# Performance work log

Hardware: AMD Instinct MI355X
Metric: run time of the kernel (lower is better)

Reference implementation:

```python
import jax, jax.numpy as jnp
import numpy as np
from jax import lax

B, C_G, H, W = 2, 64, 240, 1216
NUM, K, IDX_REF = 8, 9, 4  # prop_kernel=3
PROP_TIME = 6


def conv3x3(x, w, b):
    y = lax.conv_general_dilated(x, w, (1, 1), ((1, 1), (1, 1)),
                                 dimension_numbers=('NCHW', 'OIHW', 'NCHW'))
    return y + b[None, :, None, None]


def bilinear_sample(img, y, x):
    """img: (B,H,W); y,x: (B,K,H,W) absolute coords; zero padding outside."""
    Hh, Ww = img.shape[1], img.shape[2]
    y0 = jnp.floor(y)
    x0 = jnp.floor(x)
    wy1, wx1 = y - y0, x - x0
    gather = jax.vmap(lambda im, a, b: im[a, b])
    out = jnp.zeros_like(y)
    for i, (yy, wy) in enumerate(((y0, 1.0 - wy1), (y0 + 1.0, wy1))):
        for j, (xx, wx) in enumerate(((x0, 1.0 - wx1), (x0 + 1.0, wx1))):
            valid = (yy >= 0) & (yy <= Hh - 1) & (xx >= 0) & (xx <= Ww - 1)
            yi = jnp.clip(yy, 0, Hh - 1).astype(jnp.int32)
            xi = jnp.clip(xx, 0, Ww - 1).astype(jnp.int32)
            v = gather(img, yi, xi)
            out = out + wy * wx * jnp.where(valid, v, 0.0)
    return out


def setup_inputs() -> dict:
    key = jax.random.key(0)
    ks = jax.random.split(key, 6)
    return {
        'initial_disp': jax.random.uniform(ks[0], (B, 1, H, W), jnp.float32) * 50.0,
        'occlus_mask': jax.random.uniform(ks[1], (B, 1, H, W), jnp.float32),
        'confidence': jax.random.uniform(ks[2], (B, 1, H, W), jnp.float32),
        'guidance_feature': jax.random.normal(ks[3], (B, C_G, H, W), jnp.float32),
        'conv_w': 0.05 * jax.random.normal(ks[4], (3 * NUM, C_G, 3, 3), jnp.float32),
        'conv_b': jnp.zeros((3 * NUM,), jnp.float32),
        'aff_scale_const': jnp.full((1,), 0.5 * NUM, jnp.float32),  # TGASS: gamma*num
    }


def nlspn_forward(initial_disp, occlus_mask, confidence, guidance_feature,
                  conv_w, conv_b, aff_scale_const):
    Bb, _, Hh, Ww = guidance_feature.shape
    oa = conv3x3(guidance_feature, conv_w, conv_b)          # (B, 3*num, H, W)
    o1, o2, aff = oa[:, :NUM], oa[:, NUM:2 * NUM], oa[:, 2 * NUM:]
    off = jnp.concatenate([o1, o2], axis=1).reshape(Bb, NUM, 2, Hh, Ww)
    zero = jnp.zeros((Bb, 1, 2, Hh, Ww), off.dtype)
    off = jnp.concatenate([off[:, :IDX_REF], zero, off[:, IDX_REF:]], axis=1)  # (B,9,2,H,W)

    # TGASS affinity
    aff = jnp.tanh(aff) / (aff_scale_const[0] + 1e-8)       # (B,8,H,W)

    gy = jnp.arange(Hh, dtype=jnp.float32)[None, None, :, None]
    gx = jnp.arange(Ww, dtype=jnp.float32)[None, None, None, :]

    # confidence sampling: 1x1 deform conv (w_conf=1, bias=0), detached offsets
    off_sg = lax.stop_gradient(off)
    nb = jnp.array([0, 1, 2, 3, 5, 6, 7, 8])
    conf_s = bilinear_sample(confidence[:, 0],
                             gy + off_sg[:, nb, 0], gx + off_sg[:, nb, 1])  # (B,8,H,W)
    aff = aff * conf_s

    s = jnp.sum(jnp.abs(aff), axis=1, keepdims=True) + 1e-5
    s = jnp.where(s < 1.0, 1.0, s)
    aff = aff / s
    aff_ref = 1.0 - jnp.sum(aff, axis=1, keepdims=True)
    aff_full = jnp.concatenate([aff[:, :IDX_REF], aff_ref, aff[:, IDX_REF:]], axis=1)  # (B,9,H,W)

    # 3x3 deform conv grid (stride 1, pad 1, dil 1), weight=ones, bias=0
    kh = (jnp.arange(K) // 3 - 1).astype(jnp.float32).reshape(1, K, 1, 1)
    kw = (jnp.arange(K) % 3 - 1).astype(jnp.float32).reshape(1, K, 1, 1)
    sy = gy + kh + off[:, :, 0]
    sx = gx + kw + off[:, :, 1]

    disp = initial_disp
    list_disp = []
    for _ in range(PROP_TIME):
        samp = bilinear_sample(disp[:, 0], sy, sx)           # (B,9,H,W)
        disp = jnp.sum(aff_full * samp, axis=1, keepdims=True)
        disp = jnp.maximum(disp, 0.0)
        disp = (1.0 - occlus_mask) * disp + occlus_mask * initial_disp
        list_disp.append(disp)
    disp = jnp.maximum(disp, 0.0)

    offset_flat = off.reshape(Bb, 2 * K, Hh, Ww)
    return disp, jnp.stack(list_disp), offset_flat, aff_full, aff_scale_const


def reference(initial_disp, occlus_mask, confidence, guidance_feature,
              conv_w, conv_b, aff_scale_const):
    return nlspn_forward(initial_disp, occlus_mask, confidence, guidance_feature,
                         conv_w, conv_b, aff_scale_const)
```

## Files before the change

### kernel.cpp

```cpp
#include <hip/hip_runtime.h>
#include <hip/hip_bf16.h>
#include <math.h>
#include <string.h>

typedef __attribute__((ext_vector_type(8))) short bf16x8;
typedef __attribute__((ext_vector_type(4))) float f32x4;

constexpr int Bc = 2, CGc = 64, Hc = 240, Wc = 1216;
constexpr int IDXR = 4, PROP = 6;
constexpr long HW  = (long)Hc * Wc;
constexpr long BHW = (long)Bc * HW;

constexpr long OUT0 = 0;
constexpr long OUT1 = BHW;
constexpr long OUT2 = BHW * 7;
constexpr long OUT3 = OUT2 + (long)Bc * 18 * HW;
constexpr long OUT4 = OUT3 + (long)Bc * 9 * HW;

constexpr int HP = Hc + 2, WPAD = Wc + 2;
constexpr long APXB   = (long)HP * WPAD;
constexpr long A_TOT  = (long)Bc * APXB * 128;
constexpr long WOFF   = A_TOT;
constexpr long WS_NEED = WOFF + (long)9 * 32 * 128;

constexpr int PR = 4, PC = 64, HLO = 6;
constexpr int TR = PR + 2 * HLO;
constexpr int TC = PC + 2 * HLO + 1;

__device__ __forceinline__ unsigned short f2bf(float f) {
  __hip_bfloat16 h = __float2bfloat16(f);
  return __builtin_bit_cast(unsigned short, h);
}
__device__ __forceinline__ unsigned short f2h(float f) {
  _Float16 h = (_Float16)f;
  return __builtin_bit_cast(unsigned short, h);
}
__device__ __forceinline__ float h2f(unsigned short u) {
  return (float)__builtin_bit_cast(_Float16, u);
}

__device__ __forceinline__ void row2(const float* __restrict__ img, int yy, int x0,
                                     float& a, float& b) {
  if (yy >= 0 && yy < Hc) {
    if (x0 >= 0 && x0 < Wc - 1) {
      float2 v;
      __builtin_memcpy(&v, img + (long)yy * Wc + x0, 8);
      a = v.x; b = v.y;
    } else {
      a = (x0 >= 0 && x0 < Wc)         ? img[(long)yy * Wc + x0]     : 0.f;
      b = (x0 + 1 >= 0 && x0 + 1 < Wc) ? img[(long)yy * Wc + x0 + 1] : 0.f;
    }
  } else { a = 0.f; b = 0.f; }
}

__device__ __forceinline__ float bilin(const float* __restrict__ img, float y, float x) {
  float y0f = floorf(y), x0f = floorf(x);
  int y0 = (int)y0f, x0 = (int)x0f;
  float wy = y - y0f, wx = x - x0f;
  float v00, v01, v10, v11;
  row2(img, y0,     x0, v00, v01);
  row2(img, y0 + 1, x0, v10, v11);
  float top = v00 + wx * (v01 - v00);
  float bot = v10 + wx * (v11 - v10);
  return top + wy * (bot - top);
}

__device__ __forceinline__ float bilin_tile(
    const float (*tile)[TC], const float* __restrict__ db,
    int y0, int x0, float sy, float sx) {
  float yf = floorf(sy), xf = floorf(sx);
  int iy = (int)yf, ix = (int)xf;
  float wy = sy - yf, wx = sx - xf;
  if (iy >= y0 - HLO && iy + 1 <= y0 + PR - 1 + HLO &&
      ix >= x0 - HLO && ix + 1 <= x0 + PC - 1 + HLO) {
    int ly = iy - (y0 - HLO), lx = ix - (x0 - HLO);
    float v00 = tile[ly][lx],     v01 = tile[ly][lx + 1];
    float v10 = tile[ly + 1][lx], v11 = tile[ly + 1][lx + 1];
    float top = v00 + wx * (v01 - v00);
    float bot = v10 + wx * (v11 - v10);
    return top + wy * (bot - top);
  }
  return bilin(db, sy, sx);
}

__device__ __forceinline__ void stage_tile(
    float (*tile)[TC], const float* __restrict__ db, int y0, int x0, int tid) {
  for (int i = tid; i < TR * TC; i += 256) {
    int rr = i / TC, cc = i - rr * TC;
    int gy = y0 - HLO + rr, gx = x0 - HLO + cc;
    tile[rr][cc] = (gy >= 0 && gy < Hc && gx >= 0 && gx < Wc)
                       ? db[(long)gy * Wc + gx] : 0.f;
  }
}

__global__ __launch_bounds__(256) void nhwc_kernel(
    const float* __restrict__ g, char* __restrict__ ws) {
  __shared__ __align__(16) char tileb[64 * 132];
  const int tid = threadIdx.x;
  const int x0 = blockIdx.x * 64;
  const int y  = blockIdx.y;
  const int bz = blockIdx.z;
  const float* gb = g + (long)bz * CGc * HW + (long)y * Wc + x0;
  const int px = tid & 63, wv = tid >> 6;
#pragma unroll
  for (int k = 0; k < 16; ++k) {
    int ic = k * 4 + wv;
    float v = gb[(long)ic * HW + px];
    *reinterpret_cast<unsigned short*>(tileb + px * 132 + ic * 2) = f2bf(v);
  }
  __syncthreads();
  const int opx = tid >> 2, q = tid & 3;
  unsigned int u[8];
#pragma unroll
  for (int j = 0; j < 8; ++j)
    u[j] = *reinterpret_cast<unsigned int*>(tileb + opx * 132 + q * 32 + j * 4);
  char* dst = ws + ((long)(bz * HP + y + 1) * WPAD + x0 + 1 + opx) * 128 + q * 32;
  reinterpret_cast<uint4*>(dst)[0] = make_uint4(u[0], u[1], u[2], u[3]);
  reinterpret_cast<uint4*>(dst)[1] = make_uint4(u[4], u[5], u[6], u[7]);
}

__global__ __launch_bounds__(256) void border_kernel(char* __restrict__ ws) {
  constexpr int NB = 2 * WPAD + 2 * (HP - 2);
  long i = (long)blockIdx.x * 256 + threadIdx.x;
  if (i >= (long)Bc * NB) return;
  int bz = (int)(i / NB);
  int r  = (int)(i - (long)bz * NB);
  int py, px;
  if (r < WPAD)            { py = 0;      px = r; }
  else if (r < 2 * WPAD)   { py = HP - 1; px = r - WPAD; }
  else { int qq = r - 2 * WPAD; py = 1 + (qq >> 1); px = (qq & 1) ? (WPAD - 1) : 0; }
  char* p = ws + ((long)(bz * HP + py) * WPAD + px) * 128;
  uint4 z = make_uint4(0, 0, 0, 0);
#pragma unroll
  for (int j = 0; j < 8; ++j) reinterpret_cast<uint4*>(p)[j] = z;
}

__global__ __launch_bounds__(256) void wconv_kernel(
    const float* __restrict__ w, char* __restrict__ ws) {
  char* wd = ws + WOFF;
  int idx = blockIdx.x * 256 + threadIdx.x;
  if (idx < 24 * 64 * 9) {
    int oc = idx / 576, r = idx - oc * 576;
    int ic = r / 9, tap = r - ic * 9;
    *reinterpret_cast<unsigned short*>(wd + tap * 4096 + oc * 128 + ic * 2) = f2bf(w[idx]);
  } else if (idx < 32 * 64 * 9) {
    int i2 = idx - 24 * 64 * 9;
    int oc = 24 + i2 / 576, r = i2 % 576;
    int ic = r / 9, tap = r % 9;
    *reinterpret_cast<unsigned short*>(wd + tap * 4096 + oc * 128 + ic * 2) = 0;
  }
}

constexpr int CTILE_BYTES = 6 * 66 * 128;
constexpr int CUNITS = CTILE_BYTES / 16;
constexpr int EXST = 26;
constexpr int EXCH_BYTES = 4 * 64 * EXST * 4;
constexpr int DT_OFF = EXCH_BYTES;
constexpr int CT_OFF = DT_OFF + TR * TC * 4;

__global__ __launch_bounds__(256) void conv_fused_kernel(
    const char* __restrict__ ws, const float* __restrict__ bias,
    const float* __restrict__ conf, const float* __restrict__ scale_p,
    const float* __restrict__ occm, const float* __restrict__ initd,
    float* __restrict__ out) {
  __shared__ __align__(16) char smemA[CTILE_BYTES];
  const int tid  = threadIdx.x;
  const int lane = tid & 63, wv = tid >> 6;
  const int lrow = lane & 15, lgrp = lane >> 4;
  const int x0 = blockIdx.x * 64;
  const int y0 = blockIdx.y * 4;
  const int bz = blockIdx.z;

  const char* Abase = ws + ((long)(bz * HP + y0) * WPAD + x0) * 128;
#pragma unroll
  for (int it = 0; it < 13; ++it) {
    int u = it * 256 + tid;
    if (u < CUNITS) {
      int pxl = u >> 3, j = u & 7;
      int r = pxl / 66, col = pxl - r * 66;
      uint4 v = *reinterpret_cast<const uint4*>(
          Abase + ((long)r * WPAD + col) * 128 + j * 16);
      int ldsb = pxl * 128 + ((j ^ (col & 7)) << 4);
      *reinterpret_cast<uint4*>(smemA + ldsb) = v;
    }
  }
  __syncthreads();

  const char* Wb = ws + WOFF + (long)lrow * 128 + lgrp * 16;

  f32x4 acc[4][2];
#pragma unroll
  for (int h = 0; h < 4; ++h)
#pragma unroll
    for (int nt = 0; nt < 2; ++nt) acc[h][nt] = (f32x4){0.f, 0.f, 0.f, 0.f};

#pragma unroll
  for (int tap = 0; tap < 9; ++tap) {
    const int dy = tap / 3, dx = tap - dy * 3;
    const char* Wt = Wb + tap * 4096;
#pragma unroll
    for (int ks = 0; ks < 2; ++ks) {
      bf16x8 wf0 = *reinterpret_cast<const bf16x8*>(Wt + ks * 64);
      bf16x8 wf1 = *reinterpret_cast<const bf16x8*>(Wt + 2048 + ks * 64);
#pragma unroll
      for (int h = 0; h < 4; ++h) {
        const int colc = lrow + dx + h * 16;
        int abyte = ((wv + dy) * 66 + colc) * 128 +
                    ((((ks << 2) + lgrp) ^ (colc & 7)) << 4);
        bf16x8 af = *reinterpret_cast<const bf16x8*>(smemA + abyte);
        acc[h][0] = __builtin_amdgcn_mfma_f32_16x16x32_bf16(af, wf0, acc[h][0], 0, 0, 0);
        acc[h][1] = __builtin_amdgcn_mfma_f32_16x16x32_bf16(af, wf1, acc[h][1], 0, 0, 0);
      }
    }
  }
  __syncthreads();

  float* exch = reinterpret_cast<float*>(smemA);
  {
    const int y = y0 + wv;
#pragma unroll
    for (int h = 0; h < 4; ++h) {
      const int xx = x0 + h * 16 + lgrp * 4;
      const int lpx = h * 16 + lgrp * 4;
#pragma unroll
      for (int nt = 0; nt < 2; ++nt) {
        int oc = nt * 16 + lrow;
        if (oc >= 24) continue;
        float bv = bias[oc];
        f32x4 v = acc[h][nt];
#pragma unroll
        for (int j = 0; j < 4; ++j)
          exch[(wv * 64 + lpx + j) * EXST + oc] = v[j] + bv;
        if (oc < 16) {
          int n = oc >> 1, cd = oc & 1;
          int mm = (n < IDXR) ? n : n + 1;
          long dst = OUT2 + (long)(bz * 18 + 2 * mm + cd) * HW;
          float4 st = make_float4(v[0] + bv, v[1] + bv, v[2] + bv, v[3] + bv);
          *reinterpret_cast<float4*>(&out[dst + (long)y * Wc + xx]) = st;
        }
      }
    }
  }
  __syncthreads();

  float (*dtile)[TC] = reinterpret_cast<float (*)[TC]>(smemA + DT_OFF);
  float (*ctile)[TC] = reinterpret_cast<float (*)[TC]>(smemA + CT_OFF);
  const float* db    = initd + (long)bz * HW;
  const float* confb = conf  + (long)bz * HW;
  stage_tile(dtile, db,    y0, x0, tid);
  stage_tile(ctile, confb, y0, x0, tid);
  __syncthreads();

  const int row = tid >> 6, px = tid & 63;
  const int y = y0 + row, x = x0 + px;
  long rem = (long)y * Wc + x;
  long p = (long)bz * HW + rem;

  float ch[24];
#pragma unroll
  for (int j = 0; j < 24; ++j) ch[j] = exch[(row * 64 + px) * EXST + j];

  const float inv_scale = 1.f / (scale_p[0] + 1e-8f);
  float* off  = out + OUT2 + (long)bz * 18 * HW + rem;
  float* affp = out + OUT3 + (long)bz * 9  * HW + rem;

  float affr[9], oyr[9], oxr[9];
  float asum = 0.f;
#pragma unroll
  for (int m = 0; m < 8; m++) {
    int n = (m < IDXR) ? m : m + 1;
    float oy  = ch[2 * m];
    float ox  = ch[2 * m + 1];
    float raw = ch[16 + m];
    float avv = tanhf(raw) * inv_scale;
    float cs  = bilin_tile(ctile, confb, y0, x0, (float)y + oy, (float)x + ox);
    affr[n] = avv * cs;
    oyr[n] = oy; oxr[n] = ox;
    asum += fabsf(affr[n]);
  }
  float s = fmaxf(asum + 1e-5f, 1.0f);
  float inv_s = 1.f / s;
  float total = 0.f;
#pragma unroll
  for (int m = 0; m < 8; m++) {
    int n = (m < IDXR) ? m : m + 1;
    affr[n] *= inv_s; total += affr[n];
  }
  affr[IDXR] = 1.f - total;
  oyr[IDXR] = 0.f; oxr[IDXR] = 0.f;
#pragma unroll
  for (int n = 0; n < 9; n++) affp[(long)n * HW] = affr[n];
  off[(long)(2 * IDXR) * HW]     = 0.f;
  off[(long)(2 * IDXR + 1) * HW] = 0.f;
  if (p == 0) out[OUT4] = scale_p[0];

  float occv  = occm[p];
  float initv = db[rem];
  float acc0 = 0.f;
#pragma unroll
  for (int k = 0; k < 9; k++) {
    float sy = (float)(y + k / 3 - 1) + oyr[k];
    float sx = (float)(x + k % 3 - 1) + oxr[k];
    acc0 = fmaf(affr[k], bilin_tile(dtile, db, y0, x0, sy, sx), acc0);
  }
  acc0 = fmaxf(acc0, 0.f);
  out[OUT1 + p] = (1.f - occv) * acc0 + occv * initv;
}

__global__ __launch_bounds__(256) void prop_tab1_kernel(
    const float* __restrict__ dispPrev,
    const float* __restrict__ occ, const float* __restrict__ initd,
    float* __restrict__ out, uint4* __restrict__ tab4) {
  __shared__ float tile[TR][TC];
  const int tid = threadIdx.x;
  const int x0 = blockIdx.x * PC;
  const int y0 = blockIdx.y * PR;
  const int b  = blockIdx.z;
  const float* db = dispPrev + (long)b * HW;
  stage_tile(tile, db, y0, x0, tid);
  __syncthreads();

  const int y = y0 + (tid >> 6);
  const int x = x0 + (tid & 63);
  long rem = (long)y * Wc + x;
  long p = (long)b * HW + rem;

  const float* off  = out + OUT2 + (long)b * 18 * HW + rem;
  const float* affp = out + OUT3 + (long)b * 9  * HW + rem;

  float affv[9], oyv[9], oxv[9];
#pragma unroll
  for (int k = 0; k < 9; k++) {
    oyv[k]  = off[(long)(2 * k) * HW];
    oxv[k]  = off[(long)(2 * k + 1) * HW];
    affv[k] = affp[(long)k * HW];
  }
  float occv  = occ[p];
  float initv = initd[p];

  float acc = 0.f;
#pragma unroll
  for (int k = 0; k < 9; k++) {
    float sy = (float)(y + k / 3 - 1) + oyv[k];
    float sx = (float)(x + k % 3 - 1) + oxv[k];
    acc = fmaf(affv[k], bilin_tile(tile, db, y0, x0, sy, sx), acc);
  }
  acc = fmaxf(acc, 0.f);
  float res = (1.f - occv) * acc + occv * initv;
  out[OUT1 + (long)1 * BHW + p] = res;

  unsigned short hs[28];
#pragma unroll
  for (int k = 0; k < 9; k++) {
    hs[k] = f2h(affv[k]); hs[9 + k] = f2h(oyv[k]); hs[18 + k] = f2h(oxv[k]);
  }
  hs[27] = 0;
  unsigned u[16];
#pragma unroll
  for (int i = 0; i < 14; i++)
    u[i] = (unsigned)hs[2 * i] | ((unsigned)hs[2 * i + 1] << 16);
  u[14] = __builtin_bit_cast(unsigned, occv);
  u[15] = __builtin_bit_cast(unsigned, initv);
#pragma unroll
  for (int g = 0; g < 4; g++)
    tab4[(long)g * BHW + p] = make_uint4(u[4 * g], u[4 * g + 1], u[4 * g + 2], u[4 * g + 3]);
}

__global__ __launch_bounds__(256) void prop_tabN_kernel(
    const float* __restrict__ dispPrev, const uint4* __restrict__ tab4,
    float* __restrict__ out, int t) {
  __shared__ float tile[TR][TC];
  const int tid = threadIdx.x;
  const int x0 = blockIdx.x * PC;
  const int y0 = blockIdx.y * PR;
  const int b  = blockIdx.z;
  const float* db = dispPrev + (long)b * HW;
  stage_tile(tile, db, y0, x0, tid);
  __syncthreads();

  const int y = y0 + (tid >> 6);
  const int x = x0 + (tid & 63);
  long rem = (long)y * Wc + x;
  long p = (long)b * HW + rem;

  unsigned u[16];
#pragma unroll
  for (int g = 0; g < 4; g++) {
    uint4 q = tab4[(long)g * BHW + p];
    u[4 * g] = q.x; u[4 * g + 1] = q.y; u[4 * g + 2] = q.z; u[4 * g + 3] = q.w;
  }
  float fl[27];
#pragma unroll
  for (int i = 0; i < 27; i++) {
    unsigned w0 = u[i >> 1];
    fl[i] = h2f((unsigned short)((i & 1) ? (w0 >> 16) : (w0 & 0xffff)));
  }
  float occv  = __builtin_bit_cast(float, u[14]);
  float initv = __builtin_bit_cast(float, u[15]);

  float acc = 0.f;
#pragma unroll
  for (int k = 0; k < 9; k++) {
    float sy = (float)(y + k / 3 - 1) + fl[9 + k];
    float sx = (float)(x + k % 3 - 1) + fl[18 + k];
    acc = fmaf(fl[k], bilin_tile(tile, db, y0, x0, sy, sx), acc);
  }
  acc = fmaxf(acc, 0.f);
  float res = (1.f - occv) * acc + occv * initv;
  out[OUT1 + (long)t * BHW + p] = res;
  if (t == PROP - 1) out[OUT0 + p] = res;
}

constexpr int TY = 8, TX = 32;
constexpr int AR = TY + 2, AC = TX + 2;
constexpr int A_BYTES = AR * AC * CGc * 2;
constexpr int W_BYTES = 9 * 32 * 32 * 2;

__global__ __launch_bounds__(256) void conv_mfma_kernel(
    const float* __restrict__ g, const float* __restrict__ wsrc,
    const float* __restrict__ bias, float* __restrict__ out) {
  __shared__ __align__(16) char smemA[A_BYTES];
  __shared__ __align__(16) char smemW[W_BYTES];
  const int tid = threadIdx.x;
  const int x0 = blockIdx.x * TX;
  const int y0 = blockIdx.y * TY;
  const int bz = blockIdx.z;
  const float* gb = g + (long)bz * CGc * HW;
  for (int w = tid; w < AR * AC * 32; w += 256) {
    int c  = w % AC;
    int t2 = w / AC;
    int icp = t2 & 31;
    int r   = t2 >> 5;
    int y = y0 + r - 1, x = x0 + c - 1;
    float v0 = 0.f, v1 = 0.f;
    if (y >= 0 && y < Hc && x >= 0 && x < Wc) {
      const float* p = gb + (long)(2 * icp) * HW + (long)y * Wc + x;
      v0 = p[0]; v1 = p[HW];
    }
    unsigned int pk = (unsigned int)f2bf(v0) | ((unsigned int)f2bf(v1) << 16);
    int byte = (r * AC + c) * 128 + icp * 4;
    byte ^= (c & 7) << 4;
    *reinterpret_cast<unsigned int*>(smemA + byte) = pk;
  }
  auto stageW = [&](int hs) {
    for (int idx = tid; idx < 24 * 32 * 9; idx += 256) {
      int oc  = idx / 288;
      int r1  = idx - oc * 288;
      int icl = r1 / 9;
      int tap = r1 - icl * 9;
      float f = wsrc[idx + 288 * (oc + hs)];
      int byte = (tap * 32 + oc) * 64 + icl * 2;
      byte ^= (oc & 7) << 4;
      *reinterpret_cast<unsigned short*>(smemW + byte) = f2bf(f);
    }
  };
  stageW(0);
  __syncthreads();
  const int wid  = tid >> 6;
  const int lane = tid & 63;
  const int lrow = lane & 15;
  const int lgrp = lane >> 4;
  f32x4 acc[4][2];
#pragma unroll
  for (int m = 0; m < 4; m++)
#pragma unroll
    for (int nt = 0; nt < 2; nt++) acc[m][nt] = (f32x4){0.f, 0.f, 0.f, 0.f};
  for (int ks = 0; ks < 2; ++ks) {
    if (ks) { __syncthreads(); stageW(1); __syncthreads(); }
#pragma unroll
    for (int tap = 0; tap < 9; ++tap) {
      const int dy = tap / 3, dx = tap - dy * 3;
      int bb = (tap * 32 + lrow) * 64 + lgrp * 16;
      int bbyte0 = bb ^ ((lrow & 7) << 4);
      int bbyte1 = (bb + 16 * 64) ^ ((lrow & 7) << 4);
      bf16x8 bf0 = *reinterpret_cast<const bf16x8*>(smemW + bbyte0);
      bf16x8 bf1 = *reinterpret_cast<const bf16x8*>(smemW + bbyte1);
#pragma unroll
      for (int dr = 0; dr < 2; ++dr) {
        const int rin = 2 * wid + dr + dy;
#pragma unroll
        for (int h = 0; h < 2; ++h) {
          const int cin = h * 16 + lrow + dx;
          int abyte = ((rin * AC + cin) * 128 + ks * 64 + lgrp * 16) ^ ((cin & 7) << 4);
          bf16x8 af = *reinterpret_cast<const bf16x8*>(smemA + abyte);
          acc[dr * 2 + h][0] = __builtin_amdgcn_mfma_f32_16x16x32_bf16(af, bf0, acc[dr * 2 + h][0], 0, 0, 0);
          acc[dr * 2 + h][1] = __builtin_amdgcn_mfma_f32_16x16x32_bf16(af, bf1, acc[dr * 2 + h][1], 0, 0, 0);
        }
      }
    }
  }
#pragma unroll
  for (int dr = 0; dr < 2; ++dr) {
    const int yy = y0 + 2 * wid + dr;
#pragma unroll
    for (int h = 0; h < 2; ++h) {
      const int xx = x0 + h * 16 + lgrp * 4;
#pragma unroll
      for (int nt = 0; nt < 2; ++nt) {
        int oc = nt * 16 + lrow;
        if (oc >= 24) continue;
        float bv = bias[oc];
        long dst;
        if (oc < 16) {
          int n = oc >> 1, cd = oc & 1;
          int mm = (n < IDXR) ? n : n + 1;
          dst = OUT2 + (long)(bz * 18 + 2 * mm + cd) * HW;
        } else {
          int i2 = oc - 16;
          int mm = (i2 < IDXR) ? i2 : i2 + 1;
          dst = OUT3 + (long)(bz * 9 + mm) * HW;
        }
        f32x4 v = acc[dr * 2 + h][nt];
        float4 st = make_float4(v[0] + bv, v[1] + bv, v[2] + bv, v[3] + bv);
        *reinterpret_cast<float4*>(&out[dst + (long)yy * Wc + xx]) = st;
      }
    }
  }
}

__global__ __launch_bounds__(256) void prep_kernel(
    const float* __restrict__ conf, const float* __restrict__ scale_p,
    float* __restrict__ out) {
  long p = (long)blockIdx.x * 256 + threadIdx.x;
  if (p >= BHW) return;
  int b = (int)(p / HW);
  long rem = p - (long)b * HW;
  int y = (int)(rem / Wc);
  int x = (int)(rem - (long)y * Wc);
  const float inv_scale = 1.f / (scale_p[0] + 1e-8f);
  const float* confb = conf + (long)b * HW;
  float* off  = out + OUT2 + (long)b * 18 * HW + rem;
  float* affp = out + OUT3 + (long)b * 9  * HW + rem;
  float a[8];
  float asum = 0.f;
#pragma unroll
  for (int m = 0; m < 8; m++) {
    int n = (m < IDXR) ? m : m + 1;
    float oy  = off[(long)(2 * n) * HW];
    float ox  = off[(long)(2 * n + 1) * HW];
    float raw = affp[(long)n * HW];
    float av  = tanhf(raw) * inv_scale;
    float cs  = bilin(confb, (float)y + oy, (float)x + ox);
    a[m] = av * cs;
    asum += fabsf(a[m]);
  }
  float s = fmaxf(asum + 1e-5f, 1.0f);
  float inv_s = 1.f / s;
  float total = 0.f;
#pragma unroll
  for (int m = 0; m < 8; m++) { a[m] *= inv_s; total += a[m]; }
  float aref = 1.f - total;
#pragma unroll
  for (int m = 0; m < 8; m++) {
    int n = (m < IDXR) ? m : m + 1;
    affp[(long)n * HW] = a[m];
  }
  affp[(long)IDXR * HW] = aref;
  off[(long)(2 * IDXR) * HW]     = 0.f;
  off[(long)(2 * IDXR + 1) * HW] = 0.f;
  if (p == 0) out[OUT4] = scale_p[0];
}

__global__ __launch_bounds__(256) void prop_kernel(
    const float* __restrict__ dispPrev,
    const float* __restrict__ occ, const float* __restrict__ initd,
    float* __restrict__ out, int t) {
  long p = (long)blockIdx.x * 256 + threadIdx.x;
  if (p >= BHW) return;
  int b = (int)(p / HW);
  long rem = p - (long)b * HW;
  int y = (int)(rem / Wc);
  int x = (int)(rem - (long)y * Wc);
  const float* off  = out + OUT2 + (long)b * 18 * HW + rem;
  const float* affp = out + OUT3 + (long)b * 9  * HW + rem;
  const float* db   = dispPrev + (long)b * HW;
  float acc = 0.f;
#pragma unroll
  for (int k = 0; k < 9; k++) {
    float oy = off[(long)(2 * k) * HW];
    float ox = off[(long)(2 * k + 1) * HW];
    float av = affp[(long)k * HW];
    float sy = (float)(y + k / 3 - 1) + oy;
    float sx = (float)(x + k % 3 - 1) + ox;
    acc = fmaf(av, bilin(db, sy, sx), acc);
  }
  acc = fmaxf(acc, 0.f);
  float o = occ[p];
  float res = (1.f - o) * acc + o * initd[p];
  out[OUT1 + (long)t * BHW + p] = res;
  if (t == PROP - 1) out[OUT0 + p] = res;
}

extern "C" void kernel_launch(void* const* d_in, const int* in_sizes, int n_in,
                              void* d_out, int out_size, void* d_ws, size_t ws_size,
                              hipStream_t stream) {
  const float* initd = (const float*)d_in[0];
  const float* occ   = (const float*)d_in[1];
  const float* conf  = (const float*)d_in[2];
  const float* guid  = (const float*)d_in[3];
  const float* cw    = (const float*)d_in[4];
  const float* cb    = (const float*)d_in[5];
  const float* csc   = (const float*)d_in[6];
  float* out = (float*)d_out;
  int nblk = (int)((BHW + 255) / 256);

  if (ws_size >= (size_t)WS_NEED) {
    char* ws = (char*)d_ws;
    nhwc_kernel<<<dim3(Wc / 64, Hc, Bc), 256, 0, stream>>>(guid, ws);
    border_kernel<<<(Bc * (2 * WPAD + 2 * (HP - 2)) + 255) / 256, 256, 0, stream>>>(ws);
    wconv_kernel<<<72, 256, 0, stream>>>(cw, ws);

    dim3 pgrid(Wc / PC, Hc / PR, Bc);
    conv_fused_kernel<<<pgrid, 256, 0, stream>>>(ws, cb, conf, csc, occ, initd, out);

    uint4* tab4 = (uint4*)ws;
    prop_tab1_kernel<<<pgrid, 256, 0, stream>>>(out + OUT1, occ, initd, out, tab4);
    for (int t = 2; t < PROP; t++) {
      const float* dp = out + OUT1 + (long)(t - 1) * BHW;
      prop_tabN_kernel<<<pgrid, 256, 0, stream>>>(dp, tab4, out, t);
    }
  } else {
    conv_mfma_kernel<<<dim3(Wc / TX, Hc / TY, Bc), 256, 0, stream>>>(guid, cw, cb, out);
    prep_kernel<<<nblk, 256, 0, stream>>>(conf, csc, out);
    for (int t = 0; t < PROP; t++) {
      const float* dp = (t == 0) ? initd : (out + OUT1 + (long)(t - 1) * BHW);
      prop_kernel<<<nblk, 256, 0, stream>>>(dp, occ, initd, out, t);
    }
  }
}
```

Baseline: 201.3 us.

## Prefetch disp/conf halo tiles into registers before MFMA loop, use fast tanh

The fused conv kernel now issues global loads for the initial-disparity and confidence halo tiles before the MFMA convolution, keeping them in registers and writing them to shared memory after the exchange stores. This overlaps their latency with the matrix work and removes one barrier. It also changes the exchange stride from 26 to 33 to cut LDS bank conflicts, swaps tanhf for an exp-based approximation, and reads initv from the shared tile. The cost is extra register pressure across the MFMA loop and slightly different tanh accuracy.

```diff
diff --git a/kernel.cpp b/kernel.cpp
--- a/kernel.cpp
+++ b/kernel.cpp
@@ -37,6 +37,11 @@
 }
 __device__ __forceinline__ float h2f(unsigned short u) {
   return (float)__builtin_bit_cast(_Float16, u);
+}
+__device__ __forceinline__ float fast_tanh(float x) {
+  float xc = fminf(fmaxf(x, -15.f), 15.f);
+  float e = __expf(2.f * xc);
+  return (e - 1.f) / (e + 1.f);
 }
 
 __device__ __forceinline__ void row2(const float* __restrict__ img, int yy, int x0,
@@ -153,10 +158,11 @@
 
 constexpr int CTILE_BYTES = 6 * 66 * 128;
 constexpr int CUNITS = CTILE_BYTES / 16;
-constexpr int EXST = 26;
+constexpr int EXST = 33;
 constexpr int EXCH_BYTES = 4 * 64 * EXST * 4;
 constexpr int DT_OFF = EXCH_BYTES;
 constexpr int CT_OFF = DT_OFF + TR * TC * 4;
+constexpr int TILE_N = TR * TC;
 
 __global__ __launch_bounds__(256) void conv_fused_kernel(
     const char* __restrict__ ws, const float* __restrict__ bias,
@@ -184,6 +190,24 @@
       *reinterpret_cast<uint4*>(smemA + ldsb) = v;
     }
   }
+
+  const float* db    = initd + (long)bz * HW;
+  const float* confb = conf  + (long)bz * HW;
+  float rD[5], rC[5];
+#pragma unroll
+  for (int k = 0; k < 5; ++k) {
+    int i = k * 256 + tid;
+    rD[k] = 0.f; rC[k] = 0.f;
+    if (i < TILE_N) {
+      int rr = i / TC, cc = i - rr * TC;
+      int gy = y0 - HLO + rr, gx = x0 - HLO + cc;
+      if (gy >= 0 && gy < Hc && gx >= 0 && gx < Wc) {
+        long o = (long)gy * Wc + gx;
+        rD[k] = db[o];
+        rC[k] = confb[o];
+      }
+    }
+  }
   __syncthreads();
 
   const char* Wb = ws + WOFF + (long)lrow * 128 + lgrp * 16;
@@ -216,6 +240,8 @@
   __syncthreads();
 
   float* exch = reinterpret_cast<float*>(smemA);
+  float* dflat = reinterpret_cast<float*>(smemA + DT_OFF);
+  float* cflat = reinterpret_cast<float*>(smemA + CT_OFF);
   {
     const int y = y0 + wv;
 #pragma unroll
@@ -241,16 +267,15 @@
       }
     }
   }
+#pragma unroll
+  for (int k = 0; k < 5; ++k) {
+    int i = k * 256 + tid;
+    if (i < TILE_N) { dflat[i] = rD[k]; cflat[i] = rC[k]; }
+  }
   __syncthreads();
 
   float (*dtile)[TC] = reinterpret_cast<float (*)[TC]>(smemA + DT_OFF);
   float (*ctile)[TC] = reinterpret_cast<float (*)[TC]>(smemA + CT_OFF);
-  const float* db    = initd + (long)bz * HW;
-  const float* confb = conf  + (long)bz * HW;
-  stage_tile(dtile, db,    y0, x0, tid);
-  stage_tile(ctile, confb, y0, x0, tid);
-  __syncthreads();
-
   const int row = tid >> 6, px = tid & 63;
   const int y = y0 + row, x = x0 + px;
   long rem = (long)y * Wc + x;
@@ -272,7 +297,7 @@
     float oy  = ch[2 * m];
     float ox  = ch[2 * m + 1];
     float raw = ch[16 + m];
-    float avv = tanhf(raw) * inv_scale;
+    float avv = fast_tanh(raw) * inv_scale;
     float cs  = bilin_tile(ctile, confb, y0, x0, (float)y + oy, (float)x + ox);
     affr[n] = avv * cs;
     oyr[n] = oy; oxr[n] = ox;
@@ -295,7 +320,7 @@
   if (p == 0) out[OUT4] = scale_p[0];
 
   float occv  = occm[p];
-  float initv = db[rem];
+  float initv = dtile[HLO + row][HLO + px];
   float acc0 = 0.f;
 #pragma unroll
   for (int k = 0; k < 9; k++) {
```

Result: faster. 194.9 us, median of 2 (-3.2%).
